# Optimization experiments

Hardware: AMD Instinct MI355X
Metric: run time of the kernel (lower is better)

Reference implementation:

```python
import jax, jax.numpy as jnp
import numpy as np

EPS = 1e-6      # mLSTM normalizer epsilon
LN_EPS = 1e-5   # LayerNorm epsilon (equinox default)
S, E, NH = 2048, 1024, 8
DH = E // NH


def setup_inputs() -> dict:
    key = jax.random.key(0)
    ks = jax.random.split(key, 7)
    q = jax.random.normal(ks[0], (S, E), jnp.float32)
    k = jax.random.normal(ks[1], (S, E), jnp.float32)
    v = jax.random.normal(ks[2], (S, E), jnp.float32)
    # Gate projections: Linear(3E -> NH). Module inits weights to zero; we use
    # small random weights so the S x S gate structure is data-dependent and the
    # full math path is exercised. Biases follow the module's init scheme.
    igate_w = 0.02 * jax.random.normal(ks[3], (NH, 3 * E), jnp.float32)
    igate_b = jnp.linspace(3.0, 6.0, NH, dtype=jnp.float32)
    fgate_w = 0.02 * jax.random.normal(ks[4], (NH, 3 * E), jnp.float32)
    fgate_b = jnp.sqrt(jnp.float32(0.1)) * jax.random.normal(ks[5], (NH,), jnp.float32)
    ln_w = jnp.ones((E,), jnp.float32)  # outnorm weight (use_bias=False)
    return {"q": q, "k": k, "v": v, "igate_w": igate_w, "igate_b": igate_b,
            "fgate_w": fgate_w, "fgate_b": fgate_b, "ln_w": ln_w}


def _mlstm_forward(q, k, v, igate_w, igate_b, fgate_w, fgate_b, ln_w):
    s, e = q.shape
    nh = igate_b.shape[0]
    dh = e // nh
    # gate preactivations from concatenated q,k,v: [S, 3E] @ [3E, NH] -> [NH, S]
    x = jnp.concatenate([q, k, v], axis=1)
    ig = (x @ igate_w.T + igate_b).T            # [NH, S]
    fg = (x @ fgate_w.T + fgate_b).T            # [NH, S]
    # split heads: [NH, S, DH]
    qh = q.reshape(s, nh, dh).transpose(1, 0, 2)
    kh = k.reshape(s, nh, dh).transpose(1, 0, 2)
    vh = v.reshape(s, nh, dh).transpose(1, 0, 2)
    # log forget gates and cumulative sums (with leading zero)
    logf = jax.nn.log_sigmoid(fg)                                   # [NH, S]
    cs = jnp.concatenate([jnp.zeros((nh, 1), logf.dtype),
                          jnp.cumsum(logf, axis=1)], axis=1)        # [NH, S+1]
    # log_fg_matrix[h,i,j] = cs[h,i+1] - cs[h,j+1], masked to causal
    dlog = cs[:, 1:, None] - cs[:, None, 1:]                        # [NH, S, S]
    mask = jnp.tril(jnp.ones((s, s), dtype=bool))
    log_fg_matrix = jnp.where(mask, dlog, -jnp.inf)
    # log D = log forget decay + input gate preact (per source position j)
    log_D = log_fg_matrix + ig[:, None, :]                          # [NH, S, S]
    max_log_D = jnp.max(log_D, axis=-1, keepdims=True)              # row-wise stabilization
    D = jnp.exp(log_D - max_log_D)
    qk = jnp.einsum("hsd,htd->hst", qh, kh) / jnp.sqrt(jnp.float32(dh))
    C = qk * D
    normalizer = jnp.maximum(jnp.abs(C.sum(axis=-1, keepdims=True)), jnp.exp(-max_log_D))
    h = jnp.einsum("hst,htd->hsd", C / (normalizer + EPS), vh)      # [NH, S, DH]
    h = h.transpose(1, 0, 2).reshape(s, e)
    # outnorm: LayerNorm over embedding dim, weight only (no bias)
    mu = h.mean(axis=-1, keepdims=True)
    var = ((h - mu) ** 2).mean(axis=-1, keepdims=True)
    return (h - mu) / jnp.sqrt(var + LN_EPS) * ln_w


def reference(q, k, v, igate_w, igate_b, fgate_w, fgate_b, ln_w):
    return _mlstm_forward(q, k, v, igate_w, igate_b, fgate_w, fgate_b, ln_w)
```

## Files before the change

### kernel.cpp

```cpp
#include <hip/hip_runtime.h>
#include <hip/hip_bf16.h>
#include <math.h>

#define S_LEN 2048
#define E_DIM 1024
#define NHEAD 8
#define DHEAD 128
#define MEPS 1e-6f
#define LNEPS 1e-5f
#define TASKS_PER_HEAD 61

typedef __bf16 bf16x8 __attribute__((ext_vector_type(8)));
typedef __bf16 bf16x4 __attribute__((ext_vector_type(4)));
typedef float f32x4 __attribute__((ext_vector_type(4)));
typedef float f32x16 __attribute__((ext_vector_type(16)));

__device__ __host__ inline int ns_of(int qg) { return (4 * qg + 13) / 10; }

__device__ inline void split8(const float* x, bf16x8& hi, bf16x8& lo) {
#pragma unroll
  for (int e = 0; e < 8; ++e) {
    float v = x[e];
    __bf16 h = (__bf16)v;
    hi[e] = h;
    lo[e] = (__bf16)(v - (float)h);
  }
}

__device__ inline int cvtpk(float a, float b) {
  int d;
  asm("v_cvt_pk_bf16_f32 %0, %1, %2" : "=v"(d) : "v"(a), "v"(b));
  return d;
}

__global__ __launch_bounds__(256) void wfrag_kernel(
    const float* __restrict__ igw, const float* __restrict__ fgw,
    __bf16* __restrict__ WfH, __bf16* __restrict__ WfL) {
  int slot = blockIdx.x * 256 + threadIdx.x;
  int f = slot >> 6, l = slot & 63;
  int c = l & 15;
  int koff = f * 32 + (l >> 4) * 8;
  const float* wrow = (c < 8) ? (igw + c * 3072) : (fgw + (c - 8) * 3072);
  float buf[8];
#pragma unroll
  for (int e = 0; e < 8; ++e) buf[e] = wrow[koff + e];
  bf16x8 fh, fl; split8(buf, fh, fl);
  *(bf16x8*)(WfH + (size_t)slot * 8) = fh;
  *(bf16x8*)(WfL + (size_t)slot * 8) = fl;
}

__global__ __launch_bounds__(256) void gates_mfma_kernel(
    const float* __restrict__ q, const float* __restrict__ k, const float* __restrict__ v,
    const __bf16* __restrict__ WfH, const __bf16* __restrict__ WfL,
    float* __restrict__ gpart) {
  int rb = blockIdx.x >> 3;
  int ks = blockIdx.x & 7;
  int r0 = rb * 64;
  int tid = threadIdx.x, wave = tid >> 6, lane = tid & 63;
  int l15 = lane & 15, hi = lane >> 4;
  __shared__ char Xl[64 * 512];

  f32x4 cacc = (f32x4){0.f, 0.f, 0.f, 0.f};
  for (int ch = 0; ch < 3; ++ch) {
    int kb = ks * 384 + ch * 128;
    __syncthreads();
#pragma unroll
    for (int it = 0; it < 8; ++it) {
      int fid = it * 256 + tid;
      int row = fid >> 5, c4 = (fid & 31) * 4;
      int kk = kb + c4;
      const float* src = (kk < 1024) ? (q + (size_t)(r0 + row) * 1024 + kk)
                       : (kk < 2048) ? (k + (size_t)(r0 + row) * 1024 + (kk - 1024))
                                     : (v + (size_t)(r0 + row) * 1024 + (kk - 2048));
      float4 xv = *(const float4*)src;
      *(float4*)(Xl + ((row * 512 + c4 * 4) ^ ((row & 7) << 4))) = xv;
    }
    __syncthreads();
#pragma unroll
    for (int kc = 0; kc < 4; ++kc) {
      int row = wave * 16 + l15;
      int base = row * 512 + (kc * 32 + hi * 8) * 4;
      int x = (row & 7) << 4;
      float buf[8];
      *(float4*)&buf[0] = *(const float4*)(Xl + (base ^ x));
      *(float4*)&buf[4] = *(const float4*)(Xl + ((base + 16) ^ x));
      bf16x8 ah, al; split8(buf, ah, al);
      int gkc = ks * 12 + ch * 4 + kc;
      bf16x8 bh = *(const bf16x8*)(WfH + (size_t)(gkc * 64 + lane) * 8);
      bf16x8 bl = *(const bf16x8*)(WfL + (size_t)(gkc * 64 + lane) * 8);
      cacc = __builtin_amdgcn_mfma_f32_16x16x32_bf16(ah, bh, cacc, 0, 0, 0);
      cacc = __builtin_amdgcn_mfma_f32_16x16x32_bf16(ah, bl, cacc, 0, 0, 0);
      cacc = __builtin_amdgcn_mfma_f32_16x16x32_bf16(al, bh, cacc, 0, 0, 0);
    }
  }
#pragma unroll
  for (int rg = 0; rg < 4; ++rg) {
    int r = r0 + wave * 16 + hi * 4 + rg;
    gpart[((size_t)ks * S_LEN + r) * 16 + l15] = cacc[rg];
  }
}

__global__ __launch_bounds__(256) void combine_ls_kernel(
    const float* __restrict__ gpart, const float* __restrict__ igb,
    const float* __restrict__ fgb, float* __restrict__ ig, double* __restrict__ ls) {
  int t = blockIdx.x * 256 + threadIdx.x;
  int r = t >> 4, c = t & 15;
  float s = 0.f;
#pragma unroll
  for (int ks = 0; ks < 8; ++ks) s += gpart[((size_t)ks * S_LEN + r) * 16 + c];
  if (c < 8) {
    ig[c * S_LEN + r] = s + igb[c];
  } else {
    double x = (double)(s + fgb[c - 8]);
    ls[(c - 8) * S_LEN + r] = fmin(x, 0.0) - log1p(exp(-fabs(x)));
  }
}

__global__ void scan_kernel(const float* __restrict__ ig, const double* __restrict__ ls,
                            double* __restrict__ g, double* __restrict__ Mv,
                            float* __restrict__ rexpv) {
  int h = blockIdx.x;
  int lane = threadIdx.x;
  double cs0[32];
  const double* lsp = ls + h * S_LEN + lane * 32;
  double run = 0.0;
#pragma unroll
  for (int e = 0; e < 32; ++e) { run += lsp[e]; cs0[e] = run; }
  double incl = run;
#pragma unroll
  for (int off = 1; off < 64; off <<= 1) {
    double nb = __shfl_up(incl, off);
    if (lane >= off) incl += nb;
  }
  double base = __shfl_up(incl, 1);
  if (lane == 0) base = 0.0;
#pragma unroll
  for (int e = 0; e < 32; ++e) cs0[e] += base;

  const float* igp = ig + h * S_LEN + lane * 32;
  double gv[32];
#pragma unroll
  for (int e = 0; e < 32; ++e) {
    gv[e] = (double)igp[e] - cs0[e];
    g[h * S_LEN + lane * 32 + e] = gv[e];
  }
  double pm = -INFINITY;
#pragma unroll
  for (int e = 0; e < 32; ++e) { pm = fmax(pm, gv[e]); gv[e] = pm; }
  double inclm = pm;
#pragma unroll
  for (int off = 1; off < 64; off <<= 1) {
    double nb = __shfl_up(inclm, off);
    if (lane >= off) inclm = fmax(inclm, nb);
  }
  double basem = __shfl_up(inclm, 1);
  if (lane == 0) basem = -INFINITY;
#pragma unroll
  for (int e = 0; e < 32; ++e) {
    double Mi = fmax(basem, gv[e]);
    Mv[h * S_LEN + lane * 32 + e] = Mi;
    rexpv[h * S_LEN + lane * 32 + e] = __expf(-(float)(cs0[e] + Mi));
  }
}

__global__ __launch_bounds__(256) void rebase_kernel(
    const double* __restrict__ g, const double* __restrict__ Mv,
    float* __restrict__ gq, float* __restrict__ Mq) {
  const double L2E = 1.4426950408889634;
  int b = blockIdx.x;
  int h = b >> 4, qg = b & 15;
  int tid = threadIdx.x;
  double base = Mv[h * S_LEN + qg * 128];
#pragma unroll
  for (int it = 0; it < 8; ++it) {
    int j = it * 256 + tid;
    gq[(size_t)(h * 16 + qg) * S_LEN + j] = (float)((g[h * S_LEN + j] - base) * L2E);
  }
  if (tid < 128) {
    int i = qg * 128 + tid;
    Mq[h * S_LEN + i] = (float)((Mv[h * S_LEN + i] - base) * L2E);
  }
}

__global__ __launch_bounds__(256) void convert_kernel(
    const float* __restrict__ k, const float* __restrict__ v,
    __bf16* __restrict__ KfH, __bf16* __restrict__ KfL, __bf16* __restrict__ VT) {
  int h = blockIdx.x >> 6, kvt = blockIdx.x & 63;
  int t = threadIdx.x;
  __shared__ float Kl[32][132], Vl[32][132];
  int kvbase = kvt * 32;
#pragma unroll
  for (int it = 0; it < 4; ++it) {
    int fid = it * 256 + t;
    int r = fid >> 5, c4 = (fid & 31) * 4;
    *(float4*)&Kl[r][c4] = *(const float4*)(k + (size_t)(kvbase + r) * E_DIM + h * DHEAD + c4);
    *(float4*)&Vl[r][c4] = *(const float4*)(v + (size_t)(kvbase + r) * E_DIM + h * DHEAD + c4);
  }
  __syncthreads();
  size_t tb = (size_t)(h * 64 + kvt) * 4096;
#pragma unroll
  for (int it = 0; it < 2; ++it) {
    int slot = it * 256 + t;
    int f = slot >> 6, l = slot & 63;
    int l31 = l & 31, hi = l >> 5;
    {
      float buf[8];
#pragma unroll
      for (int e = 0; e < 8; ++e) buf[e] = Kl[l31][f * 16 + hi * 8 + e];
      bf16x8 fh, fl; split8(buf, fh, fl);
      *(bf16x8*)(KfH + tb + (size_t)slot * 8) = fh;
      *(bf16x8*)(KfL + tb + (size_t)slot * 8) = fl;
    }
    {
      int dt = f >> 1, kch = f & 1;
      bf16x8 fh;
#pragma unroll
      for (int e = 0; e < 8; ++e) fh[e] = (__bf16)Vl[kch * 16 + hi * 8 + e][dt * 32 + l31];
      *(bf16x8*)(VT + tb + (size_t)slot * 8) = fh;
    }
  }
}

__global__ __launch_bounds__(256, 2) void attn_kernel(
    const float* __restrict__ q,
    const __bf16* __restrict__ KfH, const __bf16* __restrict__ KfL,
    const __bf16* __restrict__ VT,
    const float* __restrict__ gq, const float* __restrict__ Mq,
    __bf16* __restrict__ part, float* __restrict__ bpart) {
  int rem = blockIdx.x;
  int qg = 15, preLow = 0, ns = 1;
  for (int qq = 15; qq >= 0; --qq) {
    int n = ns_of(qq);
    if (rem < 8 * n) { qg = qq; ns = n; break; }
    rem -= 8 * n;
  }
  for (int qq = 0; qq < qg; ++qq) preLow += ns_of(qq);
  int h = rem & 7;
  int split = rem >> 3;
  int T = 4 * qg + 4;
  int kb_lo = (split * T) / ns;
  int kb_hi = ((split + 1) * T) / ns;
  int Tq = kb_hi - kb_lo;
  int tid = threadIdx.x, wave = tid >> 6, lane = tid & 63;
  int l31 = lane & 31, hi = lane >> 5;
  const float scale = 0.08838834764831845f;

  __shared__ char smem[49152];

  int qrow = qg * 128 + wave * 32 + l31;
  bf16x8 qfh[8], qfl[8];
  {
    const float* qp = q + (size_t)qrow * E_DIM + h * DHEAD + hi * 8;
#pragma unroll
    for (int kch = 0; kch < 8; ++kch) {
      float buf[8];
      *(float4*)&buf[0] = *(const float4*)(qp + kch * 16);
      *(float4*)&buf[4] = *(const float4*)(qp + kch * 16 + 4);
#pragma unroll
      for (int e = 0; e < 8; ++e) buf[e] *= scale;
      split8(buf, qfh[kch], qfl[kch]);
    }
  }
  float Mreg = Mq[h * S_LEN + qrow];
  const float* gqh = gq + (size_t)(h * 16 + qg) * S_LEN;

  f32x16 acc[4];
#pragma unroll
  for (int dt = 0; dt < 4; ++dt) acc[dt] = (f32x16)(0.f);
  float bacc = 0.f;

  size_t laneoff = (size_t)lane * 8;
  auto STAGE = [&](int kb, int buf) {
    size_t tb = (size_t)(h * 64 + kb) * 4096;
    char* lb = smem + buf * 24576;
#pragma unroll
    for (int i = 0; i < 6; ++i) {
      int c = wave * 6 + i;
      const __bf16* src;
      if (c < 8)       src = KfH + tb + (size_t)c * 512 + laneoff;
      else if (c < 16) src = KfL + tb + (size_t)(c - 8) * 512 + laneoff;
      else             src = VT  + tb + (size_t)(c - 16) * 512 + laneoff;
      __builtin_amdgcn_global_load_lds(
          (const __attribute__((address_space(1))) void*)src,
          (__attribute__((address_space(3))) void*)(lb + c * 1024), 16, 0, 0);
    }
  };

  if (Tq > 0) STAGE(kb_lo, 0);
  int cur = 0;
  for (int t = 0; t < Tq; ++t) {
    int kb = kb_lo + t;
    if (t + 1 < Tq) {
      STAGE(kb + 1, cur ^ 1);
      asm volatile("s_waitcnt vmcnt(6)" ::: "memory");
    } else {
      asm volatile("s_waitcnt vmcnt(0)" ::: "memory");
    }
    __builtin_amdgcn_sched_barrier(0);
    asm volatile("s_barrier" ::: "memory");

    int qrelw = qg * 128 + wave * 32 - kb * 32;
    if (qrelw + 31 >= 0) {
      char* lb = smem + cur * 24576;
      int qrel = qrelw + l31;
      float4 g4[4];
#pragma unroll
      for (int c = 0; c < 4; ++c) g4[c] = *(const float4*)(gqh + kb * 32 + 8 * c + 4 * hi);
      f32x16 sA = (f32x16)(0.f), sB = (f32x16)(0.f), sC = (f32x16)(0.f);
      __builtin_amdgcn_s_setprio(1);
#pragma unroll
      for (int kch = 0; kch < 8; ++kch) {
        bf16x8 kh = *(const bf16x8*)(lb + kch * 1024 + lane * 16);
        bf16x8 kl = *(const bf16x8*)(lb + 8192 + kch * 1024 + lane * 16);
        sA = __builtin_amdgcn_mfma_f32_32x32x16_bf16(kh, qfh[kch], sA, 0, 0, 0);
        sB = __builtin_amdgcn_mfma_f32_32x32x16_bf16(kl, qfh[kch], sB, 0, 0, 0);
        sC = __builtin_amdgcn_mfma_f32_32x32x16_bf16(kh, qfl[kch], sC, 0, 0, 0);
      }
      __builtin_amdgcn_s_setprio(0);
      float p[16];
      float bp0 = 0.f, bp1 = 0.f, bp2 = 0.f, bp3 = 0.f;
      if (qrelw >= 31) {
#pragma unroll
        for (int rg = 0; rg < 16; ++rg) {
          float sv = sA[rg] + sB[rg] + sC[rg];
          p[rg] = sv * exp2f(((const float*)&g4[rg >> 2])[rg & 3] - Mreg);
          if ((rg & 3) == 0) bp0 += p[rg];
          else if ((rg & 3) == 1) bp1 += p[rg];
          else if ((rg & 3) == 2) bp2 += p[rg];
          else bp3 += p[rg];
        }
      } else {
#pragma unroll
        for (int rg = 0; rg < 16; ++rg) {
          int J = (rg & 3) + 8 * (rg >> 2) + 4 * hi;
          float sv = sA[rg] + sB[rg] + sC[rg];
          float w = sv * exp2f(((const float*)&g4[rg >> 2])[rg & 3] - Mreg);
          p[rg] = (J <= qrel) ? w : 0.f;
          if ((rg & 3) == 0) bp0 += p[rg];
          else if ((rg & 3) == 1) bp1 += p[rg];
          else if ((rg & 3) == 2) bp2 += p[rg];
          else bp3 += p[rg];
        }
      }
      bacc += (bp0 + bp1) + (bp2 + bp3);
#pragma unroll
      for (int kch = 0; kch < 2; ++kch) {
        const float* pp = p + kch * 8;
        int a0 = cvtpk(pp[0], pp[1]);
        int a1 = cvtpk(pp[2], pp[3]);
        int a2 = cvtpk(pp[4], pp[5]);
        int a3 = cvtpk(pp[6], pp[7]);
        asm("v_permlane32_swap_b32 %0, %1" : "+v"(a0), "+v"(a2));
        asm("v_permlane32_swap_b32 %0, %1" : "+v"(a1), "+v"(a3));
        union { int w[4]; bf16x8 v; } pb;
        pb.w[0] = a0; pb.w[1] = a1; pb.w[2] = a2; pb.w[3] = a3;
        __builtin_amdgcn_s_setprio(1);
#pragma unroll
        for (int dt = 0; dt < 4; ++dt) {
          bf16x8 va = *(const bf16x8*)(lb + 16384 + (dt * 2 + kch) * 1024 + lane * 16);
          acc[dt] = __builtin_amdgcn_mfma_f32_32x32x16_bf16(va, pb.v, acc[dt], 0, 0, 0);
        }
        __builtin_amdgcn_s_setprio(0);
      }
    }
    asm volatile("s_barrier" ::: "memory");
    cur ^= 1;
  }

  {
    int x = __float_as_int(bacc), y = x;
    asm("v_permlane32_swap_b32 %0, %1" : "+v"(x), "+v"(y));
    float bfull = __int_as_float(x) + __int_as_float(y);
    int task = h * TASKS_PER_HEAD + preLow + split;
    if (lane < 32) bpart[task * 128 + wave * 32 + lane] = bfull;

    __syncthreads();
    char* Tls = smem + wave * 8704;
#pragma unroll
    for (int dt = 0; dt < 4; ++dt)
#pragma unroll
      for (int rgq = 0; rgq < 4; ++rgq) {
        bf16x4 pk;
        pk[0] = (__bf16)acc[dt][rgq * 4 + 0];
        pk[1] = (__bf16)acc[dt][rgq * 4 + 1];
        pk[2] = (__bf16)acc[dt][rgq * 4 + 2];
        pk[3] = (__bf16)acc[dt][rgq * 4 + 3];
        int d0 = dt * 32 + rgq * 8 + hi * 4;
        *(bf16x4*)(Tls + l31 * 272 + d0 * 2) = pk;
      }
    __syncthreads();
    __bf16* pp = part + (size_t)task * 16384;
#pragma unroll
    for (int it = 0; it < 8; ++it) {
      int qr = it * 4 + (lane >> 4);
      int chunk = lane & 15;
      bf16x8 vrow = *(const bf16x8*)(Tls + qr * 272 + chunk * 16);
      *(bf16x8*)(pp + ((size_t)(wave * 32 + qr) * 128 + chunk * 8)) = vrow;
    }
  }
}

__global__ __launch_bounds__(256) void cln_kernel(
    const __bf16* __restrict__ part, const float* __restrict__ bpart,
    const float* __restrict__ rexpv, const float* __restrict__ lnw,
    float* __restrict__ out) {
  int b = blockIdx.x;
  int qg = b >> 4, slab = b & 15;
  int ns = ns_of(qg);
  int preLow = 0;
  for (int qq = 0; qq < qg; ++qq) preLow += ns_of(qq);
  int tid = threadIdx.x;
  int tokl = tid >> 5;
  int j = tid & 31;
  int qv = slab * 8 + tokl;
  int tok = qg * 128 + qv;
  int h = j >> 2;
  int d0 = (j & 3) * 32;
  int task0 = h * TASKS_PER_HEAD + preLow;

  float a[32];
#pragma unroll
  for (int i = 0; i < 32; ++i) a[i] = 0.f;
  float bb = 0.f;
  for (int s = 0; s < ns; ++s) {
    const __bf16* pp = part + (size_t)(task0 + s) * 16384 + qv * 128 + d0;
#pragma unroll
    for (int c = 0; c < 4; ++c) {
      bf16x8 xv = *(const bf16x8*)(pp + c * 8);
#pragma unroll
      for (int e = 0; e < 8; ++e) a[c * 8 + e] += (float)xv[e];
    }
    bb += bpart[(task0 + s) * 128 + qv];
  }
  float norm = fmaxf(fabsf(bb), rexpv[h * S_LEN + tok]) + MEPS;
  float inv = 1.f / norm;
  float sum = 0.f, sq = 0.f;
#pragma unroll
  for (int i = 0; i < 32; ++i) {
    a[i] *= inv;
    sum += a[i];
    sq += a[i] * a[i];
  }
#pragma unroll
  for (int off = 1; off < 32; off <<= 1) {
    sum += __shfl_xor(sum, off);
    sq  += __shfl_xor(sq, off);
  }
  float mu = sum * (1.f / E_DIM);
  float var = sq * (1.f / E_DIM) - mu * mu;
  float rstd = rsqrtf(var + LNEPS);
  float* dst = out + (size_t)tok * E_DIM + j * 32;
  const float* wsrc = lnw + j * 32;
#pragma unroll
  for (int c = 0; c < 8; ++c) {
    float4 w = *(const float4*)(wsrc + c * 4);
    float4 o;
    o.x = (a[c * 4 + 0] - mu) * rstd * w.x;
    o.y = (a[c * 4 + 1] - mu) * rstd * w.y;
    o.z = (a[c * 4 + 2] - mu) * rstd * w.z;
    o.w = (a[c * 4 + 3] - mu) * rstd * w.w;
    *(float4*)(dst + c * 4) = o;
  }
}

extern "C" void kernel_launch(void* const* d_in, const int* in_sizes, int n_in,
                              void* d_out, int out_size, void* d_ws, size_t ws_size,
                              hipStream_t stream) {
  const float* q   = (const float*)d_in[0];
  const float* k   = (const float*)d_in[1];
  const float* v   = (const float*)d_in[2];
  const float* igw = (const float*)d_in[3];
  const float* igb = (const float*)d_in[4];
  const float* fgw = (const float*)d_in[5];
  const float* fgb = (const float*)d_in[6];
  const float* lnw = (const float*)d_in[7];
  float* out = (float*)d_out;

  const size_t MB = 1024 * 1024;
  char* base = (char*)d_ws;
  float*  ig    = (float*)(base + 0);
  float*  rexpv = (float*)(base + 64 * 1024);
  float*  Mq    = (float*)(base + 128 * 1024);
  float*  bpart = (float*)(base + 192 * 1024);
  double* ls    = (double*)(base + 704 * 1024);
  double* g64   = (double*)(base + 832 * 1024);
  double* M64   = (double*)(base + 960 * 1024);
  __bf16* WfH   = (__bf16*)(base + 1088 * 1024);
  __bf16* WfL   = (__bf16*)(base + 1184 * 1024);
  float*  gq    = (float*)(base + 1536 * 1024);
  __bf16* KfH   = (__bf16*)(base + 3 * MB);
  __bf16* KfL   = (__bf16*)(base + 7 * MB);
  __bf16* VT    = (__bf16*)(base + 11 * MB);
  __bf16* part  = (__bf16*)(base + 15 * MB);
  float*  gpart = (float*)(base + 31 * MB);

  int nblocks = 8 * TASKS_PER_HEAD;

  wfrag_kernel<<<dim3(24), dim3(256), 0, stream>>>(igw, fgw, WfH, WfL);
  convert_kernel<<<dim3(512), dim3(256), 0, stream>>>(k, v, KfH, KfL, VT);
  gates_mfma_kernel<<<dim3(256), dim3(256), 0, stream>>>(q, k, v, WfH, WfL, gpart);
  combine_ls_kernel<<<dim3(128), dim3(256), 0, stream>>>(gpart, igb, fgb, ig, ls);
  scan_kernel<<<dim3(NHEAD), dim3(64), 0, stream>>>(ig, ls, g64, M64, rexpv);
  rebase_kernel<<<dim3(128), dim3(256), 0, stream>>>(g64, M64, gq, Mq);
  attn_kernel<<<dim3(nblocks), dim3(256), 0, stream>>>(q, KfH, KfL, VT, gq, Mq, part, bpart);
  cln_kernel<<<dim3(256), dim3(256), 0, stream>>>(part, bpart, rexpv, lnw, out);
}
```

Before: 80.36 us.

## Fuse preprocessing kernels and rebalance attention split-K task counts

After: 86.16 us. +7.2%, slower.

```diff
diff --git a/kernel.cpp b/kernel.cpp
--- a/kernel.cpp
+++ b/kernel.cpp
@@ -8,14 +8,14 @@
 #define DHEAD 128
 #define MEPS 1e-6f
 #define LNEPS 1e-5f
-#define TASKS_PER_HEAD 61
+#define TASKS_PER_HEAD 96
 
 typedef __bf16 bf16x8 __attribute__((ext_vector_type(8)));
 typedef __bf16 bf16x4 __attribute__((ext_vector_type(4)));
 typedef float f32x4 __attribute__((ext_vector_type(4)));
 typedef float f32x16 __attribute__((ext_vector_type(16)));
 
-__device__ __host__ inline int ns_of(int qg) { return (4 * qg + 13) / 10; }
+__device__ __host__ inline int ns_of(int qg) { return (4 * qg + 9) / 6; }
 
 __device__ inline void split8(const float* x, bf16x8& hi, bf16x8& lo) {
 #pragma unroll
@@ -33,20 +33,59 @@
   return d;
 }
 
-__global__ __launch_bounds__(256) void wfrag_kernel(
+__global__ __launch_bounds__(256) void convw_kernel(
+    const float* __restrict__ k, const float* __restrict__ v,
     const float* __restrict__ igw, const float* __restrict__ fgw,
+    __bf16* __restrict__ KfH, __bf16* __restrict__ KfL, __bf16* __restrict__ VT,
     __bf16* __restrict__ WfH, __bf16* __restrict__ WfL) {
-  int slot = blockIdx.x * 256 + threadIdx.x;
-  int f = slot >> 6, l = slot & 63;
-  int c = l & 15;
-  int koff = f * 32 + (l >> 4) * 8;
-  const float* wrow = (c < 8) ? (igw + c * 3072) : (fgw + (c - 8) * 3072);
-  float buf[8];
-#pragma unroll
-  for (int e = 0; e < 8; ++e) buf[e] = wrow[koff + e];
-  bf16x8 fh, fl; split8(buf, fh, fl);
-  *(bf16x8*)(WfH + (size_t)slot * 8) = fh;
-  *(bf16x8*)(WfL + (size_t)slot * 8) = fl;
+  __shared__ float Kl[32][132], Vl[32][132];
+  int t = threadIdx.x;
+  if (blockIdx.x >= 512) {
+    int slot = (blockIdx.x - 512) * 256 + t;
+    int f = slot >> 6, l = slot & 63;
+    int c = l & 15;
+    int koff = f * 32 + (l >> 4) * 8;
+    const float* wrow = (c < 8) ? (igw + c * 3072) : (fgw + (c - 8) * 3072);
+    float buf[8];
+#pragma unroll
+    for (int e = 0; e < 8; ++e) buf[e] = wrow[koff + e];
+    bf16x8 fh, fl; split8(buf, fh, fl);
+    *(bf16x8*)(WfH + (size_t)slot * 8) = fh;
+    *(bf16x8*)(WfL + (size_t)slot * 8) = fl;
+    return;
+  }
+  int h = blockIdx.x >> 6, kvt = blockIdx.x & 63;
+  int kvbase = kvt * 32;
+#pragma unroll
+  for (int it = 0; it < 4; ++it) {
+    int fid = it * 256 + t;
+    int r = fid >> 5, c4 = (fid & 31) * 4;
+    *(float4*)&Kl[r][c4] = *(const float4*)(k + (size_t)(kvbase + r) * E_DIM + h * DHEAD + c4);
+    *(float4*)&Vl[r][c4] = *(const float4*)(v + (size_t)(kvbase + r) * E_DIM + h * DHEAD + c4);
+  }
+  __syncthreads();
+  size_t tb = (size_t)(h * 64 + kvt) * 4096;
+#pragma unroll
+  for (int it = 0; it < 2; ++it) {
+    int slot = it * 256 + t;
+    int f = slot >> 6, l = slot & 63;
+    int l31 = l & 31, hi = l >> 5;
+    {
+      float buf[8];
+#pragma unroll
+      for (int e = 0; e < 8; ++e) buf[e] = Kl[l31][f * 16 + hi * 8 + e];
+      bf16x8 fh, fl; split8(buf, fh, fl);
+      *(bf16x8*)(KfH + tb + (size_t)slot * 8) = fh;
+      *(bf16x8*)(KfL + tb + (size_t)slot * 8) = fl;
+    }
+    {
+      int dt = f >> 1, kch = f & 1;
+      bf16x8 fh;
+#pragma unroll
+      for (int e = 0; e < 8; ++e) fh[e] = (__bf16)Vl[kch * 16 + hi * 8 + e][dt * 32 + l31];
+      *(bf16x8*)(VT + tb + (size_t)slot * 8) = fh;
+    }
+  }
 }
 
 __global__ __launch_bounds__(256) void gates_mfma_kernel(
@@ -100,123 +139,89 @@
   }
 }
 
-__global__ __launch_bounds__(256) void combine_ls_kernel(
-    const float* __restrict__ gpart, const float* __restrict__ igb,
-    const float* __restrict__ fgb, float* __restrict__ ig, double* __restrict__ ls) {
-  int t = blockIdx.x * 256 + threadIdx.x;
-  int r = t >> 4, c = t & 15;
-  float s = 0.f;
-#pragma unroll
-  for (int ks = 0; ks < 8; ++ks) s += gpart[((size_t)ks * S_LEN + r) * 16 + c];
-  if (c < 8) {
-    ig[c * S_LEN + r] = s + igb[c];
-  } else {
-    double x = (double)(s + fgb[c - 8]);
-    ls[(c - 8) * S_LEN + r] = fmin(x, 0.0) - log1p(exp(-fabs(x)));
-  }
-}
-
-__global__ void scan_kernel(const float* __restrict__ ig, const double* __restrict__ ls,
-                            double* __restrict__ g, double* __restrict__ Mv,
-                            float* __restrict__ rexpv) {
+__global__ __launch_bounds__(256) void gatepost_kernel(
+    const float* __restrict__ gpart, const float* __restrict__ igb, const float* __restrict__ fgb,
+    float* __restrict__ gq, float* __restrict__ Mq, float* __restrict__ rexpv) {
   int h = blockIdx.x;
-  int lane = threadIdx.x;
-  double cs0[32];
-  const double* lsp = ls + h * S_LEN + lane * 32;
-  double run = 0.0;
-#pragma unroll
-  for (int e = 0; e < 32; ++e) { run += lsp[e]; cs0[e] = run; }
-  double incl = run;
-#pragma unroll
-  for (int off = 1; off < 64; off <<= 1) {
-    double nb = __shfl_up(incl, off);
-    if (lane >= off) incl += nb;
-  }
-  double base = __shfl_up(incl, 1);
-  if (lane == 0) base = 0.0;
-#pragma unroll
-  for (int e = 0; e < 32; ++e) cs0[e] += base;
-
-  const float* igp = ig + h * S_LEN + lane * 32;
-  double gv[32];
-#pragma unroll
-  for (int e = 0; e < 32; ++e) {
-    gv[e] = (double)igp[e] - cs0[e];
-    g[h * S_LEN + lane * 32 + e] = gv[e];
-  }
-  double pm = -INFINITY;
-#pragma unroll
-  for (int e = 0; e < 32; ++e) { pm = fmax(pm, gv[e]); gv[e] = pm; }
-  double inclm = pm;
-#pragma unroll
-  for (int off = 1; off < 64; off <<= 1) {
-    double nb = __shfl_up(inclm, off);
-    if (lane >= off) inclm = fmax(inclm, nb);
-  }
-  double basem = __shfl_up(inclm, 1);
-  if (lane == 0) basem = -INFINITY;
-#pragma unroll
-  for (int e = 0; e < 32; ++e) {
-    double Mi = fmax(basem, gv[e]);
-    Mv[h * S_LEN + lane * 32 + e] = Mi;
-    rexpv[h * S_LEN + lane * 32 + e] = __expf(-(float)(cs0[e] + Mi));
-  }
-}
-
-__global__ __launch_bounds__(256) void rebase_kernel(
-    const double* __restrict__ g, const double* __restrict__ Mv,
-    float* __restrict__ gq, float* __restrict__ Mq) {
+  int tid = threadIdx.x;
+  __shared__ double Lls[2048];
+  __shared__ float  Lig[2048];
+  __shared__ double Lg[2048];
+  __shared__ double Lcs[2048];
+  __shared__ double LM[2048];
+
+  float bi = igb[h], bf = fgb[h];
+#pragma unroll
+  for (int it = 0; it < 8; ++it) {
+    int r = it * 256 + tid;
+    float si = 0.f, sf = 0.f;
+#pragma unroll
+    for (int ks = 0; ks < 8; ++ks) {
+      const float* gp = gpart + ((size_t)ks * S_LEN + r) * 16;
+      si += gp[h];
+      sf += gp[h + 8];
+    }
+    Lig[r] = si + bi;
+    double x = (double)(sf + bf);
+    Lls[r] = fmin(x, 0.0) - log1p(exp(-fabs(x)));
+  }
+  __syncthreads();
+
+  if (tid < 64) {
+    int lane = tid;
+    double cs0[32];
+    double run = 0.0;
+#pragma unroll
+    for (int e = 0; e < 32; ++e) { run += Lls[lane * 32 + e]; cs0[e] = run; }
+    double incl = run;
+#pragma unroll
+    for (int off = 1; off < 64; off <<= 1) {
+      double nb = __shfl_up(incl, off);
+      if (lane >= off) incl += nb;
+    }
+    double base = __shfl_up(incl, 1);
+    if (lane == 0) base = 0.0;
+#pragma unroll
+    for (int e = 0; e < 32; ++e) cs0[e] += base;
+
+    double gv[32];
+#pragma unroll
+    for (int e = 0; e < 32; ++e) {
+      gv[e] = (double)Lig[lane * 32 + e] - cs0[e];
+      Lg[lane * 32 + e] = gv[e];
+      Lcs[lane * 32 + e] = cs0[e];
+    }
+    double pm = -INFINITY;
+#pragma unroll
+    for (int e = 0; e < 32; ++e) { pm = fmax(pm, gv[e]); gv[e] = pm; }
+    double inclm = pm;
+#pragma unroll
+    for (int off = 1; off < 64; off <<= 1) {
+      double nb = __shfl_up(inclm, off);
+      if (lane >= off) inclm = fmax(inclm, nb);
+    }
+    double basem = __shfl_up(inclm, 1);
+    if (lane == 0) basem = -INFINITY;
+#pragma unroll
+    for (int e = 0; e < 32; ++e) LM[lane * 32 + e] = fmax(basem, gv[e]);
+  }
+  __syncthreads();
+
   const double L2E = 1.4426950408889634;
-  int b = blockIdx.x;
-  int h = b >> 4, qg = b & 15;
-  int tid = threadIdx.x;
-  double base = Mv[h * S_LEN + qg * 128];
 #pragma unroll
   for (int it = 0; it < 8; ++it) {
-    int j = it * 256 + tid;
-    gq[(size_t)(h * 16 + qg) * S_LEN + j] = (float)((g[h * S_LEN + j] - base) * L2E);
-  }
-  if (tid < 128) {
-    int i = qg * 128 + tid;
-    Mq[h * S_LEN + i] = (float)((Mv[h * S_LEN + i] - base) * L2E);
-  }
-}
-
-__global__ __launch_bounds__(256) void convert_kernel(
-    const float* __restrict__ k, const float* __restrict__ v,
-    __bf16* __restrict__ KfH, __bf16* __restrict__ KfL, __bf16* __restrict__ VT) {
-  int h = blockIdx.x >> 6, kvt = blockIdx.x & 63;
-  int t = threadIdx.x;
-  __shared__ float Kl[32][132], Vl[32][132];
-  int kvbase = kvt * 32;
-#pragma unroll
-  for (int it = 0; it < 4; ++it) {
-    int fid = it * 256 + t;
-    int r = fid >> 5, c4 = (fid & 31) * 4;
-    *(float4*)&Kl[r][c4] = *(const float4*)(k + (size_t)(kvbase + r) * E_DIM + h * DHEAD + c4);
-    *(float4*)&Vl[r][c4] = *(const float4*)(v + (size_t)(kvbase + r) * E_DIM + h * DHEAD + c4);
-  }
-  __syncthreads();
-  size_t tb = (size_t)(h * 64 + kvt) * 4096;
-#pragma unroll
-  for (int it = 0; it < 2; ++it) {
-    int slot = it * 256 + t;
-    int f = slot >> 6, l = slot & 63;
-    int l31 = l & 31, hi = l >> 5;
-    {
-      float buf[8];
-#pragma unroll
-      for (int e = 0; e < 8; ++e) buf[e] = Kl[l31][f * 16 + hi * 8 + e];
-      bf16x8 fh, fl; split8(buf, fh, fl);
-      *(bf16x8*)(KfH + tb + (size_t)slot * 8) = fh;
-      *(bf16x8*)(KfL + tb + (size_t)slot * 8) = fl;
-    }
-    {
-      int dt = f >> 1, kch = f & 1;
-      bf16x8 fh;
-#pragma unroll
-      for (int e = 0; e < 8; ++e) fh[e] = (__bf16)Vl[kch * 16 + hi * 8 + e][dt * 32 + l31];
-      *(bf16x8*)(VT + tb + (size_t)slot * 8) = fh;
+    int i = it * 256 + tid;
+    int qgi = i >> 7;
+    Mq[h * S_LEN + i] = (float)((LM[i] - LM[qgi * 128]) * L2E);
+    rexpv[h * S_LEN + i] = __expf(-(float)(Lcs[i] + LM[i]));
+  }
+  for (int qg = 0; qg < 16; ++qg) {
+    double base = LM[qg * 128];
+    float* dst = gq + (size_t)(h * 16 + qg) * S_LEN;
+#pragma unroll
+    for (int it = 0; it < 8; ++it) {
+      int j = it * 256 + tid;
+      dst[j] = (float)((Lg[j] - base) * L2E);
     }
   }
 }
@@ -478,13 +483,9 @@
 
   const size_t MB = 1024 * 1024;
   char* base = (char*)d_ws;
-  float*  ig    = (float*)(base + 0);
   float*  rexpv = (float*)(base + 64 * 1024);
   float*  Mq    = (float*)(base + 128 * 1024);
   float*  bpart = (float*)(base + 192 * 1024);
-  double* ls    = (double*)(base + 704 * 1024);
-  double* g64   = (double*)(base + 832 * 1024);
-  double* M64   = (double*)(base + 960 * 1024);
   __bf16* WfH   = (__bf16*)(base + 1088 * 1024);
   __bf16* WfL   = (__bf16*)(base + 1184 * 1024);
   float*  gq    = (float*)(base + 1536 * 1024);
@@ -492,16 +493,13 @@
   __bf16* KfL   = (__bf16*)(base + 7 * MB);
   __bf16* VT    = (__bf16*)(base + 11 * MB);
   __bf16* part  = (__bf16*)(base + 15 * MB);
-  float*  gpart = (float*)(base + 31 * MB);
+  float*  gpart = (float*)(base + 39 * MB);
 
   int nblocks = 8 * TASKS_PER_HEAD;
 
-  wfrag_kernel<<<dim3(24), dim3(256), 0, stream>>>(igw, fgw, WfH, WfL);
-  convert_kernel<<<dim3(512), dim3(256), 0, stream>>>(k, v, KfH, KfL, VT);
+  convw_kernel<<<dim3(536), dim3(256), 0, stream>>>(k, v, igw, fgw, KfH, KfL, VT, WfH, WfL);
   gates_mfma_kernel<<<dim3(256), dim3(256), 0, stream>>>(q, k, v, WfH, WfL, gpart);
-  combine_ls_kernel<<<dim3(128), dim3(256), 0, stream>>>(gpart, igb, fgb, ig, ls);
-  scan_kernel<<<dim3(NHEAD), dim3(64), 0, stream>>>(ig, ls, g64, M64, rexpv);
-  rebase_kernel<<<dim3(128), dim3(256), 0, stream>>>(g64, M64, gq, Mq);
+  gatepost_kernel<<<dim3(NHEAD), dim3(256), 0, stream>>>(gpart, igb, fgb, gq, Mq, rexpv);
   attn_kernel<<<dim3(nblocks), dim3(256), 0, stream>>>(q, KfH, KfL, VT, gq, Mq, part, bpart);
   cln_kernel<<<dim3(256), dim3(256), 0, stream>>>(part, bpart, rexpv, lnw, out);
 }
```
